# Kernel optimization log

Hardware: AMD Instinct MI355X
Metric: run time of the kernel (lower is better)

Reference implementation:

```python
import jax, jax.numpy as jnp
import numpy as np

SEQ_LEN = 512
VOCAB = 32000
EMB = 512
HID = 1024
NUM_CLASSES = 32000
BATCH = 64


def _lstm_layer(x, w_ih, w_hh, b_ih, b_hh):
    # x: [B, T, D_in]; PyTorch gate order i, f, g, o; weights [4H, D]
    B = x.shape[0]
    H = w_hh.shape[1]
    # precompute input projections for all timesteps: [T, B, 4H]
    xg = jnp.einsum('btd,gd->tbg', x, w_ih) + (b_ih + b_hh)

    def step(carry, xt):
        h, c = carry
        gates = xt + h @ w_hh.T  # [B, 4H]
        i, f, g, o = jnp.split(gates, 4, axis=-1)
        i = jax.nn.sigmoid(i)
        f = jax.nn.sigmoid(f)
        g = jnp.tanh(g)
        o = jax.nn.sigmoid(o)
        c = f * c + i * g
        h = o * jnp.tanh(c)
        return (h, c), h

    h0 = jnp.zeros((B, H), dtype=x.dtype)
    c0 = jnp.zeros((B, H), dtype=x.dtype)
    _, hs = jax.lax.scan(step, (h0, c0), xg)  # hs: [T, B, H]
    return jnp.transpose(hs, (1, 0, 2))  # [B, T, H]


def setup_inputs() -> dict:
    key = jax.random.key(0)
    ks = jax.random.split(key, 12)
    s_e = 1.0 / np.sqrt(EMB)
    s_h = 1.0 / np.sqrt(HID)
    inp = {
        'features': jax.random.randint(ks[0], (BATCH, SEQ_LEN), 0, VOCAB, dtype=jnp.int64)
            if jax.config.jax_enable_x64 else jax.random.randint(ks[0], (BATCH, SEQ_LEN), 0, VOCAB, dtype=jnp.int32),
        'emb': jax.random.normal(ks[1], (VOCAB + 1, EMB), jnp.float32),
        'w_ih0': jax.random.uniform(ks[2], (4 * HID, EMB), jnp.float32, -s_h, s_h),
        'w_hh0': jax.random.uniform(ks[3], (4 * HID, HID), jnp.float32, -s_h, s_h),
        'b_ih0': jax.random.uniform(ks[4], (4 * HID,), jnp.float32, -s_h, s_h),
        'b_hh0': jax.random.uniform(ks[5], (4 * HID,), jnp.float32, -s_h, s_h),
        'w_ih1': jax.random.uniform(ks[6], (4 * HID, HID), jnp.float32, -s_h, s_h),
        'w_hh1': jax.random.uniform(ks[7], (4 * HID, HID), jnp.float32, -s_h, s_h),
        'b_ih1': jax.random.uniform(ks[8], (4 * HID,), jnp.float32, -s_h, s_h),
        'b_hh1': jax.random.uniform(ks[9], (4 * HID,), jnp.float32, -s_h, s_h),
        'fc_w': jax.random.uniform(ks[10], (NUM_CLASSES, HID), jnp.float32, -s_h, s_h),
        'fc_b': jax.random.uniform(ks[11], (NUM_CLASSES,), jnp.float32, -s_h, s_h),
    }
    return inp


def reference(features, emb, w_ih0, w_hh0, b_ih0, b_hh0,
              w_ih1, w_hh1, b_ih1, b_hh1, fc_w, fc_b):
    # seq_lens = sum(features != vocab_size - 1) - 1
    seq_lens = jnp.sum(features != (VOCAB - 1), axis=1) - 1  # [B]
    x = emb[features]  # [B, T, E]
    h1 = _lstm_layer(x, w_ih0, w_hh0, b_ih0, b_hh0)   # [B, T, H]
    h2 = _lstm_layer(h1, w_ih1, w_hh1, b_ih1, b_hh1)  # [B, T, H]
    # gather output at seq_lens per batch row
    last = jnp.take_along_axis(h2, seq_lens[:, None, None].astype(jnp.int32), axis=1)[:, 0]  # [B, H]
    # dropout_rate = 0.0 -> identity
    pred = last @ fc_w.T + fc_b  # [B, num_classes]
    return pred
```

## Files before the change

kernel.cpp:

```cpp
#include <hip/hip_runtime.h>

#define NWG   256
#define NTHR  512
#define TSEQ  512
#define HID   1024
#define NCLS  32000
#define KP1   2056
#define KP0   1544
#define RP    44
#define F0IDX 288
#define F1IDX 608
#define SPIN_GUARD 50000000u

typedef __attribute__((ext_vector_type(8))) short short8;
typedef __attribute__((ext_vector_type(4))) float floatx4;

struct AB { short8 a[4]; short8 b[2]; };

__device__ __forceinline__ unsigned short f2bf(float f) {
  union { float f; unsigned u; } c; c.f = f;
  unsigned r = c.u + 0x7fffu + ((c.u >> 16) & 1u);
  return (unsigned short)(r >> 16);
}
__device__ __forceinline__ float sigmoidf_(float x) {
  x = fminf(30.f, fmaxf(-30.f, x));
  return 1.f / (1.f + __expf(-x));
}
__device__ __forceinline__ float tanhf_(float x) {
  x = fminf(15.f, fmaxf(-15.f, x));
  float e = __expf(2.f * x);
  return (e - 1.f) / (e + 1.f);
}
__device__ __forceinline__ void st_u32_agent(unsigned* p, unsigned v) {
  __hip_atomic_store(p, v, __ATOMIC_RELAXED, __HIP_MEMORY_SCOPE_AGENT);
}

__device__ __forceinline__ void mfma8(const AB& f, floatx4 (&acc)[4][2]) {
#pragma unroll
  for (int mt = 0; mt < 4; ++mt)
#pragma unroll
    for (int nt = 0; nt < 2; ++nt)
      acc[mt][nt] = __builtin_amdgcn_mfma_f32_16x16x32_bf16(f.a[mt], f.b[nt], acc[mt][nt], 0, 0, 0);
}

template <int NKT, int KPAD>
__device__ __forceinline__ void gemm_part(
    int kb, int keo, int lm,
    const unsigned short* const (&ab)[4],
    const unsigned short* wl, floatx4 (&acc)[4][2])
{
  AB f0, f1;
  auto ld = [&](AB& f, int kt) {
    const int off = kb + kt * 32 + keo;
#pragma unroll
    for (int nt = 0; nt < 2; ++nt)
      f.b[nt] = *reinterpret_cast<const short8*>(wl + (nt * 16 + lm) * KPAD + off);
#pragma unroll
    for (int mt = 0; mt < 4; ++mt)
      f.a[mt] = *reinterpret_cast<const short8*>(ab[mt] + off);
  };
  ld(f0, 0);
#pragma unroll
  for (int kt = 0; kt + 2 < NKT; kt += 2) {
    ld(f1, kt + 1);
    mfma8(f0, acc);
    ld(f0, kt + 2);
    mfma8(f1, acc);
  }
  ld(f1, NKT - 1);
  mfma8(f0, acc);
  mfma8(f1, acc);
}

__global__ void __launch_bounds__(NTHR, 1)
lstm_kernel(const int* __restrict__ feat,
            const float* __restrict__ emb,
            const float* __restrict__ wih0, const float* __restrict__ whh0,
            const float* __restrict__ bih0, const float* __restrict__ bhh0,
            const float* __restrict__ wih1, const float* __restrict__ whh1,
            const float* __restrict__ bih1, const float* __restrict__ bhh1,
            const float* __restrict__ fcw, const float* __restrict__ fcb,
            float* __restrict__ out,
            unsigned* __restrict__ bar)
{
  const int tid  = threadIdx.x;
  const int wg   = blockIdx.x;
  const int wave = tid >> 6;
  const int lane = tid & 63;
  const int quad = lane >> 4;
  const int lm   = lane & 15;
  const int keo  = quad * 8;

  unsigned short* sc   = (unsigned short*)out;
  unsigned short* h0   = sc;
  unsigned short* h1   = sc + 524288;
  unsigned short* lh   = sc + 655360;
  unsigned short* xbuf = sc + 720896;

  const int layer = (wg >= 128) ? 1 : 0;
  const int wl_id = wg & 127;
  const int jb = wl_id * 8;

  __shared__ unsigned short wlds[32 * KP1];
  __shared__ float red[4][32][RP];
  __shared__ int   sl[64];
  __shared__ unsigned sdone[2];

  if (tid < 2) sdone[tid] = 0;

  {
    const float* wih = layer ? wih1 : wih0;
    const float* whh = layer ? whh1 : whh0;
    const int KX   = layer ? 1024 : 512;
    const int KTOT = layer ? 2048 : 1536;
    const int KPAD = layer ? KP1 : KP0;
    for (int r = 0; r < 32; ++r) {
      const int gr = (r >> 3) * HID + jb + (r & 7);
      for (int e4 = tid; e4 < (KTOT >> 2); e4 += NTHR) {
        const int k = e4 * 4;
        float4 v = (k < KX) ? *(const float4*)(wih + (size_t)gr * KX + k)
                            : *(const float4*)(whh + (size_t)gr * 1024 + (k - KX));
        ushort4 u; u.x = f2bf(v.x); u.y = f2bf(v.y); u.z = f2bf(v.z); u.w = f2bf(v.w);
        *(ushort4*)(wlds + r * KPAD + k) = u;
      }
    }
    if (layer && tid < 64) {
      int cnt = 0;
      const int* fr = feat + tid * TSEQ;
      for (int k = 0; k < TSEQ; k += 4)
        cnt += (fr[k] != 31999) + (fr[k + 1] != 31999) +
               (fr[k + 2] != 31999) + (fr[k + 3] != 31999);
      int v = cnt - 1; if (v < 0) v = 0;
      sl[tid] = v;
    }
  }
  __syncthreads();

  float bsum[4];
  float cv[2] = {0.f, 0.f};
  int   slv[2] = {0, 0};
  const int jl_c = tid & 7;
  const int bl_c = tid >> 3;
  if (tid < 256) {
    const float* bih = layer ? bih1 : bih0;
    const float* bhh = layer ? bhh1 : bhh0;
    const int gj = jb + jl_c;
#pragma unroll
    for (int g = 0; g < 4; ++g) bsum[g] = bih[g * HID + gj] + bhh[g * HID + gj];
    if (layer) { slv[0] = sl[bl_c]; slv[1] = sl[32 + bl_c]; }
  }

  auto spin_ge = [&](int idx, unsigned need) -> unsigned {
    unsigned g = 0, v;
    while ((v = __hip_atomic_load(&bar[idx], __ATOMIC_RELAXED, __HIP_MEMORY_SCOPE_AGENT)) < need) {
      __builtin_amdgcn_s_sleep(1);
      if (++g > SPIN_GUARD) break;
    }
    return v;
  };

  auto reduce_cell = [&](floatx4 (&acc)[4][2], unsigned short* hw, int t) {
#pragma unroll
    for (int h = 0; h < 2; ++h) {
      if (wave < 4) {
#pragma unroll
        for (int mi = 0; mi < 2; ++mi)
#pragma unroll
          for (int nt = 0; nt < 2; ++nt)
#pragma unroll
            for (int r = 0; r < 4; ++r)
              red[wave][mi * 16 + quad * 4 + r][nt * 16 + lm] = acc[2 * h + mi][nt][r];
      }
      __syncthreads();
      if (wave >= 4) {
#pragma unroll
        for (int mi = 0; mi < 2; ++mi)
#pragma unroll
          for (int nt = 0; nt < 2; ++nt)
#pragma unroll
            for (int r = 0; r < 4; ++r)
              red[wave - 4][mi * 16 + quad * 4 + r][nt * 16 + lm] += acc[2 * h + mi][nt][r];
      }
      __syncthreads();
      if (tid < 256) {
        const int b = h * 32 + bl_c;
        float g0 = bsum[0], g1 = bsum[1], g2 = bsum[2], g3 = bsum[3];
#pragma unroll
        for (int v = 0; v < 4; ++v) {
          g0 += red[v][bl_c][jl_c];
          g1 += red[v][bl_c][8 + jl_c];
          g2 += red[v][bl_c][16 + jl_c];
          g3 += red[v][bl_c][24 + jl_c];
        }
        const float ig = sigmoidf_(g0);
        const float fg = sigmoidf_(g1);
        const float gg = tanhf_(g2);
        const float og = sigmoidf_(g3);
        const float cn = fg * cv[h] + ig * gg;
        cv[h] = cn;
        const float hn = og * tanhf_(cn);
        unsigned my = f2bf(hn);
        unsigned ov = (unsigned)__shfl_xor((int)my, 1, 64);
        if ((tid & 1) == 0) {
          const unsigned packed = my | (ov << 16);
          st_u32_agent((unsigned*)(hw + b * HID + jb + jl_c), packed);
          if (layer && t == slv[h])
            st_u32_agent((unsigned*)(lh + b * HID + jb + jl_c), packed);
        }
      }
      if (h == 0) __syncthreads();
    }
  };

  auto finish_step = [&](int par, unsigned r, int cbase, int c2, int cflag) {
    if (wave < 4) {
      __builtin_amdgcn_s_waitcnt(0);
      if (lane == 0)
        __hip_atomic_fetch_add(&sdone[par], 1u, __ATOMIC_RELAXED, __HIP_MEMORY_SCOPE_WORKGROUP);
    } else if (wave == 7 && lane == 0) {
      unsigned g = 0;
      while (__hip_atomic_load(&sdone[par], __ATOMIC_RELAXED, __HIP_MEMORY_SCOPE_WORKGROUP) < 4u)
        if (++g > SPIN_GUARD) break;
      __hip_atomic_store(&sdone[par], 0u, __ATOMIC_RELAXED, __HIP_MEMORY_SCOPE_WORKGROUP);
      unsigned old = __hip_atomic_fetch_add(&bar[cbase + (wg & 7) * 32], 1u,
                                            __ATOMIC_RELAXED, __HIP_MEMORY_SCOPE_AGENT);
      if (old == r * 16u - 1u) {
        unsigned mo = __hip_atomic_fetch_add(&bar[c2], 1u,
                                             __ATOMIC_RELAXED, __HIP_MEMORY_SCOPE_AGENT);
        if (mo == r * 8u - 1u)
          __hip_atomic_store(&bar[cflag], r, __ATOMIC_RELAXED, __HIP_MEMORY_SCOPE_AGENT);
      }
    }
  };

  if (!layer) {
    if (tid < 256) {
      const int b = wl_id >> 1;
      const int off = (wl_id & 1) * 256 + tid;
#pragma unroll
      for (int tt = 0; tt < 2; ++tt) {
        unsigned xv = f2bf(emb[(size_t)feat[b * TSEQ + tt] * 512 + off]);
        unsigned ov = (unsigned)__shfl_xor((int)xv, 1, 64);
        if ((tid & 1) == 0)
          st_u32_agent((unsigned*)(xbuf + tt * 32768 + b * 512 + off), xv | (ov << 16));
      }
    }
    __builtin_amdgcn_s_waitcnt(0);
    __syncthreads();
    if (tid == 0) {
      unsigned old = __hip_atomic_fetch_add(&bar[(wg & 7) * 32], 1u,
                                            __ATOMIC_RELAXED, __HIP_MEMORY_SCOPE_AGENT);
      if (old == 15u) {
        unsigned mo = __hip_atomic_fetch_add(&bar[256], 1u,
                                             __ATOMIC_RELAXED, __HIP_MEMORY_SCOPE_AGENT);
        if (mo == 7u)
          __hip_atomic_store(&bar[F0IDX], 1u, __ATOMIC_RELAXED, __HIP_MEMORY_SCOPE_AGENT);
      }
      spin_ge(F0IDX, 1u);
      __builtin_amdgcn_fence(__ATOMIC_ACQUIRE, "agent");
    }
    __syncthreads();

    unsigned seenOwn = 1, seenRing = 0;
    for (int t = 0; t < TSEQ; ++t) {
      if (t + 2 < TSEQ && tid < 256) {
        const int b = wl_id >> 1;
        const int off = (wl_id & 1) * 256 + tid;
        unsigned xv = f2bf(emb[(size_t)feat[b * TSEQ + (t + 2)] * 512 + off]);
        unsigned ov = (unsigned)__shfl_xor((int)xv, 1, 64);
        if ((tid & 1) == 0)
          st_u32_agent((unsigned*)(xbuf + ((t + 2) & 3) * 32768 + b * 512 + off), xv | (ov << 16));
      }

      floatx4 acc[4][2];
#pragma unroll
      for (int mt = 0; mt < 4; ++mt)
#pragma unroll
        for (int nt = 0; nt < 2; ++nt)
          acc[mt][nt] = (floatx4){0.f, 0.f, 0.f, 0.f};

      {
        const unsigned short* ab[4];
        const unsigned short* xq = xbuf + (size_t)(t & 3) * 32768;
#pragma unroll
        for (int mt = 0; mt < 4; ++mt) ab[mt] = xq + (mt * 16 + lm) * 512;
        gemm_part<2, KP0>(wave * 64, keo, lm, ab, wlds, acc);
      }

      if (tid == 0) {
        bool fen = false;
        const unsigned needO = (unsigned)(t + 1);
        if (seenOwn < needO) { seenOwn = spin_ge(F0IDX, needO); fen = true; }
        if (t >= 8) {
          const unsigned nr = (unsigned)(t - 7);
          if (seenRing < nr) seenRing = spin_ge(F1IDX, nr);
        }
        if (fen) __builtin_amdgcn_fence(__ATOMIC_ACQUIRE, "agent");
      }
      __syncthreads();

      {
        const unsigned short* hb[4];
        const unsigned short* h0r = h0 + (size_t)((t + 7) & 7) * 65536;
#pragma unroll
        for (int mt = 0; mt < 4; ++mt) hb[mt] = h0r + (mt * 16 + lm) * HID - 512;
        gemm_part<4, KP0>(512 + wave * 128, keo, lm, hb, wlds, acc);
      }

      reduce_cell(acc, h0 + (size_t)(t & 7) * 65536, t);
      finish_step(t & 1, (unsigned)(t + 2), 0, 256, F0IDX);
    }
  } else {
    unsigned seenX = 0;
    unsigned seenOwn = 0;
    for (int t = 0; t < TSEQ; ++t) {
      const unsigned needX = (unsigned)(t + 2);
      if (seenX < needX) {
        unsigned v = 0;
        if (lane == 0) v = spin_ge(F0IDX, needX);
        v = (unsigned)__shfl((int)v, 0, 64);
        seenX = v;
        __builtin_amdgcn_fence(__ATOMIC_ACQUIRE, "agent");
      }

      floatx4 acc[4][2];
#pragma unroll
      for (int mt = 0; mt < 4; ++mt)
#pragma unroll
        for (int nt = 0; nt < 2; ++nt)
          acc[mt][nt] = (floatx4){0.f, 0.f, 0.f, 0.f};

      {
        const unsigned short* ab[4];
        const unsigned short* h0r = h0 + (size_t)(t & 7) * 65536;
#pragma unroll
        for (int mt = 0; mt < 4; ++mt) ab[mt] = h0r + (mt * 16 + lm) * HID;
        gemm_part<4, KP1>(wave * 128, keo, lm, ab, wlds, acc);
      }

      if (tid == 0) {
        const unsigned needO = (unsigned)t;
        if (seenOwn < needO) {
          seenOwn = spin_ge(F1IDX, needO);
          __builtin_amdgcn_fence(__ATOMIC_ACQUIRE, "agent");
        }
      }
      __syncthreads();

      {
        const unsigned short* hb[4];
        const unsigned short* h1r = h1 + (size_t)((t + 1) & 1) * 65536;
#pragma unroll
        for (int mt = 0; mt < 4; ++mt) hb[mt] = h1r + (mt * 16 + lm) * HID - 1024;
        gemm_part<4, KP1>(1024 + wave * 128, keo, lm, hb, wlds, acc);
      }

      reduce_cell(acc, h1 + (size_t)(t & 1) * 65536, t);
      finish_step(t & 1, (unsigned)(t + 1), 320, 576, F1IDX);
    }
  }

  auto sync_all = [&](unsigned r) {
    __builtin_amdgcn_s_waitcnt(0);
    __syncthreads();
    if (tid == 0) {
      unsigned old = __hip_atomic_fetch_add(&bar[640 + (wg & 7) * 32], 1u,
                                            __ATOMIC_RELAXED, __HIP_MEMORY_SCOPE_AGENT);
      if (old == r * 32u - 1u) {
        unsigned mo = __hip_atomic_fetch_add(&bar[896], 1u,
                                             __ATOMIC_RELAXED, __HIP_MEMORY_SCOPE_AGENT);
        if (mo == r * 8u - 1u)
          __hip_atomic_store(&bar[928], r, __ATOMIC_RELAXED, __HIP_MEMORY_SCOPE_AGENT);
      }
      spin_ge(928, r);
      __builtin_amdgcn_fence(__ATOMIC_ACQUIRE, "agent");
    }
    __syncthreads();
  };

  sync_all(1);

  const int colbase = wg * 125;
  const int col  = colbase + wave * 16 + lm;
  const int colc = (col < NCLS) ? col : (NCLS - 1);
  floatx4 facc[4];
  {
    const unsigned short* ab[4];
#pragma unroll
    for (int mt = 0; mt < 4; ++mt) ab[mt] = lh + (mt * 16 + lm) * HID;
    const float* bb = fcw + (size_t)colc * HID;

#pragma unroll
    for (int mt = 0; mt < 4; ++mt) facc[mt] = (floatx4){0.f, 0.f, 0.f, 0.f};

    short8 a0[4], a1[4], b0, b1;
    auto ld = [&](short8 (&A)[4], short8& B, int kbase) {
      const int off = kbase + keo;
      float4 v0 = *(const float4*)(bb + off);
      float4 v1 = *(const float4*)(bb + off + 4);
      short8 bv;
      bv[0] = (short)f2bf(v0.x); bv[1] = (short)f2bf(v0.y);
      bv[2] = (short)f2bf(v0.z); bv[3] = (short)f2bf(v0.w);
      bv[4] = (short)f2bf(v1.x); bv[5] = (short)f2bf(v1.y);
      bv[6] = (short)f2bf(v1.z); bv[7] = (short)f2bf(v1.w);
      B = bv;
#pragma unroll
      for (int mt = 0; mt < 4; ++mt)
        A[mt] = *reinterpret_cast<const short8*>(ab[mt] + off);
    };
    ld(a0, b0, 0);
#pragma unroll
    for (int kt = 0; kt < 30; kt += 2) {
      ld(a1, b1, (kt + 1) * 32);
#pragma unroll
      for (int mt = 0; mt < 4; ++mt)
        facc[mt] = __builtin_amdgcn_mfma_f32_16x16x32_bf16(a0[mt], b0, facc[mt], 0, 0, 0);
      ld(a0, b0, (kt + 2) * 32);
#pragma unroll
      for (int mt = 0; mt < 4; ++mt)
        facc[mt] = __builtin_amdgcn_mfma_f32_16x16x32_bf16(a1[mt], b1, facc[mt], 0, 0, 0);
    }
    ld(a1, b1, 31 * 32);
#pragma unroll
    for (int mt = 0; mt < 4; ++mt)
      facc[mt] = __builtin_amdgcn_mfma_f32_16x16x32_bf16(a0[mt], b0, facc[mt], 0, 0, 0);
#pragma unroll
    for (int mt = 0; mt < 4; ++mt)
      facc[mt] = __builtin_amdgcn_mfma_f32_16x16x32_bf16(a1[mt], b1, facc[mt], 0, 0, 0);
  }

  sync_all(2);

  if (col < colbase + 125) {
    const float bias = fcb[col];
#pragma unroll
    for (int mt = 0; mt < 4; ++mt)
#pragma unroll
      for (int r = 0; r < 4; ++r) {
        const int row = mt * 16 + quad * 4 + r;
        out[(size_t)row * NCLS + col] = facc[mt][r] + bias;
      }
  }
}

extern "C" void kernel_launch(void* const* d_in, const int* in_sizes, int n_in,
                              void* d_out, int out_size, void* d_ws, size_t ws_size,
                              hipStream_t stream) {
  (void)in_sizes; (void)n_in; (void)out_size; (void)ws_size;
  const int*   feat = (const int*)d_in[0];
  const float* emb  = (const float*)d_in[1];
  const float* wih0 = (const float*)d_in[2];
  const float* whh0 = (const float*)d_in[3];
  const float* bih0 = (const float*)d_in[4];
  const float* bhh0 = (const float*)d_in[5];
  const float* wih1 = (const float*)d_in[6];
  const float* whh1 = (const float*)d_in[7];
  const float* bih1 = (const float*)d_in[8];
  const float* bhh1 = (const float*)d_in[9];
  const float* fcw  = (const float*)d_in[10];
  const float* fcb  = (const float*)d_in[11];
  float*       out  = (float*)d_out;
  unsigned*    bar  = (unsigned*)d_ws;

  hipMemsetAsync(d_out, 0, 1703936, stream);
  hipMemsetAsync(d_ws, 0, 8192, stream);

  void* args[] = { &feat, &emb, &wih0, &whh0, &bih0, &bhh0, &wih1, &whh1,
                   &bih1, &bhh1, &fcw, &fcb, &out, &bar };
  hipLaunchCooperativeKernel((const void*)lstm_kernel, dim3(NWG), dim3(NTHR),
                             args, 0, stream);
}
```

Before: 6.074 ms.

## Replace hierarchical atomic counter barriers with per-workgroup progress flags scanned by a wave

Each workgroup now publishes its step progress with a plain store to its own slot, instead of doing a two-level atomic fetch-add tree that ends in a single flag. Waiters use a whole wave to load all 128 per-workgroup slots and reduce them to a minimum. This is meant to remove the serialized atomic RMW chain and the extra flag hop from the critical path of every recurrent timestep. The cost is more polling traffic, since each waiter reads 128 words instead of one, and the spin guards are tightened.

```diff
diff --git a/kernel.cpp b/kernel.cpp
--- a/kernel.cpp
+++ b/kernel.cpp
@@ -8,9 +8,14 @@
 #define KP1   2056
 #define KP0   1544
 #define RP    44
-#define F0IDX 288
-#define F1IDX 608
-#define SPIN_GUARD 50000000u
+#define PROG0 256
+#define PROG1 1024
+#define FJBASE 1600
+#define FJL2   1856
+#define FJFLAG 1888
+#define SPIN_GUARD 10000000u
+#define SCAN_GUARD 1000000u
+#define SATUR 0x7FFFFFFFu
 
 typedef __attribute__((ext_vector_type(8))) short short8;
 typedef __attribute__((ext_vector_type(4))) float floatx4;
@@ -33,6 +38,9 @@
 }
 __device__ __forceinline__ void st_u32_agent(unsigned* p, unsigned v) {
   __hip_atomic_store(p, v, __ATOMIC_RELAXED, __HIP_MEMORY_SCOPE_AGENT);
+}
+__device__ __forceinline__ unsigned ld_u32_agent(const unsigned* p) {
+  return __hip_atomic_load(p, __ATOMIC_RELAXED, __HIP_MEMORY_SCOPE_AGENT);
 }
 
 __device__ __forceinline__ void mfma8(const AB& f, floatx4 (&acc)[4][2]) {
@@ -150,13 +158,54 @@
     if (layer) { slv[0] = sl[bl_c]; slv[1] = sl[32 + bl_c]; }
   }
 
-  auto spin_ge = [&](int idx, unsigned need) -> unsigned {
-    unsigned g = 0, v;
-    while ((v = __hip_atomic_load(&bar[idx], __ATOMIC_RELAXED, __HIP_MEMORY_SCOPE_AGENT)) < need) {
+  auto scan1 = [&](int base, unsigned need) -> unsigned {
+    unsigned g = 0, a0, a1;
+    bool dead = false;
+    for (;;) {
+      a0 = ld_u32_agent(&bar[base + lane * 4]);
+      a1 = ld_u32_agent(&bar[base + (64 + lane) * 4]);
+      if (__all(a0 >= need && a1 >= need)) break;
+      __builtin_amdgcn_s_sleep(1);
+      if (++g > SCAN_GUARD) { dead = true; break; }
+    }
+    if (dead) return SATUR;
+    unsigned m = a0 < a1 ? a0 : a1;
+#pragma unroll
+    for (int off = 32; off; off >>= 1) {
+      unsigned o = (unsigned)__shfl_xor((int)m, off, 64);
+      m = o < m ? o : m;
+    }
+    return m;
+  };
+  auto scan2 = [&](int baseA, unsigned needA, int baseB, unsigned needB,
+                   unsigned& minA, unsigned& minB) {
+    unsigned g = 0, a0, a1, b0, b1;
+    bool dead = false;
+    for (;;) {
+      a0 = ld_u32_agent(&bar[baseA + lane * 4]);
+      a1 = ld_u32_agent(&bar[baseA + (64 + lane) * 4]);
+      b0 = ld_u32_agent(&bar[baseB + lane * 4]);
+      b1 = ld_u32_agent(&bar[baseB + (64 + lane) * 4]);
+      if (__all(a0 >= needA && a1 >= needA && b0 >= needB && b1 >= needB)) break;
+      __builtin_amdgcn_s_sleep(1);
+      if (++g > SCAN_GUARD) { dead = true; break; }
+    }
+    if (dead) { minA = SATUR; minB = SATUR; return; }
+    unsigned ma = a0 < a1 ? a0 : a1;
+    unsigned mb = b0 < b1 ? b0 : b1;
+#pragma unroll
+    for (int off = 32; off; off >>= 1) {
+      unsigned oa = (unsigned)__shfl_xor((int)ma, off, 64); ma = oa < ma ? oa : ma;
+      unsigned ob = (unsigned)__shfl_xor((int)mb, off, 64); mb = ob < mb ? ob : mb;
+    }
+    minA = ma; minB = mb;
+  };
+  auto spin_ge = [&](int idx, unsigned need) {
+    unsigned g = 0;
+    while (ld_u32_agent(&bar[idx]) < need) {
       __builtin_amdgcn_s_sleep(1);
       if (++g > SPIN_GUARD) break;
     }
-    return v;
   };
 
   auto reduce_cell = [&](floatx4 (&acc)[4][2], unsigned short* hw, int t) {
@@ -212,7 +261,7 @@
     }
   };
 
-  auto finish_step = [&](int par, unsigned r, int cbase, int c2, int cflag) {
+  auto finish_step = [&](int par, unsigned r, int pbase) {
     if (wave < 4) {
       __builtin_amdgcn_s_waitcnt(0);
       if (lane == 0)
@@ -222,14 +271,7 @@
       while (__hip_atomic_load(&sdone[par], __ATOMIC_RELAXED, __HIP_MEMORY_SCOPE_WORKGROUP) < 4u)
         if (++g > SPIN_GUARD) break;
       __hip_atomic_store(&sdone[par], 0u, __ATOMIC_RELAXED, __HIP_MEMORY_SCOPE_WORKGROUP);
-      unsigned old = __hip_atomic_fetch_add(&bar[cbase + (wg & 7) * 32], 1u,
-                                            __ATOMIC_RELAXED, __HIP_MEMORY_SCOPE_AGENT);
-      if (old == r * 16u - 1u) {
-        unsigned mo = __hip_atomic_fetch_add(&bar[c2], 1u,
-                                             __ATOMIC_RELAXED, __HIP_MEMORY_SCOPE_AGENT);
-        if (mo == r * 8u - 1u)
-          __hip_atomic_store(&bar[cflag], r, __ATOMIC_RELAXED, __HIP_MEMORY_SCOPE_AGENT);
-      }
+      st_u32_agent(&bar[pbase + wl_id * 4], r);
     }
   };
 
@@ -247,21 +289,14 @@
     }
     __builtin_amdgcn_s_waitcnt(0);
     __syncthreads();
-    if (tid == 0) {
-      unsigned old = __hip_atomic_fetch_add(&bar[(wg & 7) * 32], 1u,
-                                            __ATOMIC_RELAXED, __HIP_MEMORY_SCOPE_AGENT);
-      if (old == 15u) {
-        unsigned mo = __hip_atomic_fetch_add(&bar[256], 1u,
-                                             __ATOMIC_RELAXED, __HIP_MEMORY_SCOPE_AGENT);
-        if (mo == 7u)
-          __hip_atomic_store(&bar[F0IDX], 1u, __ATOMIC_RELAXED, __HIP_MEMORY_SCOPE_AGENT);
-      }
-      spin_ge(F0IDX, 1u);
+    if (wave == 7 && lane == 0) st_u32_agent(&bar[PROG0 + wl_id * 4], 1u);
+    unsigned seenOwn = 1, seenRing = 0;
+    if (wave == 0) {
+      seenOwn = scan1(PROG0, 1u);
       __builtin_amdgcn_fence(__ATOMIC_ACQUIRE, "agent");
     }
     __syncthreads();
 
-    unsigned seenOwn = 1, seenRing = 0;
     for (int t = 0; t < TSEQ; ++t) {
       if (t + 2 < TSEQ && tid < 256) {
         const int b = wl_id >> 1;
@@ -287,15 +322,13 @@
         gemm_part<2, KP0>(wave * 64, keo, lm, ab, wlds, acc);
       }
 
-      if (tid == 0) {
-        bool fen = false;
+      if (wave == 0) {
         const unsigned needO = (unsigned)(t + 1);
-        if (seenOwn < needO) { seenOwn = spin_ge(F0IDX, needO); fen = true; }
-        if (t >= 8) {
-          const unsigned nr = (unsigned)(t - 7);
-          if (seenRing < nr) seenRing = spin_ge(F1IDX, nr);
+        const unsigned needR = (t >= 8) ? (unsigned)(t - 7) : 0u;
+        if (seenOwn < needO || seenRing < needR) {
+          scan2(PROG0, needO, PROG1, needR, seenOwn, seenRing);
+          __builtin_amdgcn_fence(__ATOMIC_ACQUIRE, "agent");
         }
-        if (fen) __builtin_amdgcn_fence(__ATOMIC_ACQUIRE, "agent");
       }
       __syncthreads();
 
@@ -308,7 +341,7 @@
       }
 
       reduce_cell(acc, h0 + (size_t)(t & 7) * 65536, t);
-      finish_step(t & 1, (unsigned)(t + 2), 0, 256, F0IDX);
+      finish_step(t & 1, (unsigned)(t + 2), PROG0);
     }
   } else {
     unsigned seenX = 0;
@@ -316,10 +349,7 @@
     for (int t = 0; t < TSEQ; ++t) {
       const unsigned needX = (unsigned)(t + 2);
       if (seenX < needX) {
-        unsigned v = 0;
-        if (lane == 0) v = spin_ge(F0IDX, needX);
-        v = (unsigned)__shfl((int)v, 0, 64);
-        seenX = v;
+        seenX = scan1(PROG0, needX);
         __builtin_amdgcn_fence(__ATOMIC_ACQUIRE, "agent");
       }
 
@@ -338,10 +368,10 @@
         gemm_part<4, KP1>(wave * 128, keo, lm, ab, wlds, acc);
       }
 
-      if (tid == 0) {
+      if (wave == 0) {
         const unsigned needO = (unsigned)t;
         if (seenOwn < needO) {
-          seenOwn = spin_ge(F1IDX, needO);
+          seenOwn = scan1(PROG1, needO);
           __builtin_amdgcn_fence(__ATOMIC_ACQUIRE, "agent");
         }
       }
@@ -356,7 +386,7 @@
       }
 
       reduce_cell(acc, h1 + (size_t)(t & 1) * 65536, t);
-      finish_step(t & 1, (unsigned)(t + 1), 320, 576, F1IDX);
+      finish_step(t & 1, (unsigned)(t + 1), PROG1);
     }
   }
 
@@ -364,15 +394,15 @@
     __builtin_amdgcn_s_waitcnt(0);
     __syncthreads();
     if (tid == 0) {
-      unsigned old = __hip_atomic_fetch_add(&bar[640 + (wg & 7) * 32], 1u,
+      unsigned old = __hip_atomic_fetch_add(&bar[FJBASE + (wg & 7) * 32], 1u,
                                             __ATOMIC_RELAXED, __HIP_MEMORY_SCOPE_AGENT);
       if (old == r * 32u - 1u) {
-        unsigned mo = __hip_atomic_fetch_add(&bar[896], 1u,
+        unsigned mo = __hip_atomic_fetch_add(&bar[FJL2], 1u,
                                              __ATOMIC_RELAXED, __HIP_MEMORY_SCOPE_AGENT);
         if (mo == r * 8u - 1u)
-          __hip_atomic_store(&bar[928], r, __ATOMIC_RELAXED, __HIP_MEMORY_SCOPE_AGENT);
-      }
-      spin_ge(928, r);
+          __hip_atomic_store(&bar[FJFLAG], r, __ATOMIC_RELAXED, __HIP_MEMORY_SCOPE_AGENT);
+      }
+      spin_ge(FJFLAG, r);
       __builtin_amdgcn_fence(__ATOMIC_ACQUIRE, "agent");
     }
     __syncthreads();
```

After: 5.842 ms. -3.8%, faster.
